# Kernel optimization log

Hardware: AMD Instinct MI355X
Metric: run time of the kernel (lower is better)

## Reference

```python
import jax, jax.numpy as jnp
import numpy as np

NUM_HEADS = 16
NUM_KV_HEADS = 4
FEATURES = 2048
HEAD_DIM = 128
SOFT_CAP = 50.0
WINDOW = 1024
B, T = 2, 2048


def apply_rope(inputs, positions, head_dim, max_wavelength=10000):
    # inputs: [B, T, N, H], positions: [B, T]
    fraction = 2 * jnp.arange(0, head_dim // 2) / head_dim
    timescale = max_wavelength ** fraction  # [H/2]
    sinusoid = positions[..., jnp.newaxis] / timescale[jnp.newaxis, jnp.newaxis, :]  # [B,T,H/2]
    sinusoid = sinusoid[..., jnp.newaxis, :]  # [B,T,1,H/2]
    sin, cos = jnp.sin(sinusoid), jnp.cos(sinusoid)
    first, second = jnp.split(inputs, 2, axis=-1)
    out = jnp.concatenate([first * cos - second * sin, second * cos + first * sin], axis=-1)
    return out.astype(inputs.dtype)


def setup_inputs() -> dict:
    key = jax.random.key(0)
    k1, k2, k3, k4 = jax.random.split(key, 4)
    x = jax.random.normal(k1, (B, T, FEATURES), dtype=jnp.float32)
    segment_pos = jnp.tile(jnp.arange(T, dtype=jnp.int32)[None, :], (B, 1))
    attn_mask = jnp.tril(jnp.ones((T, T), dtype=bool))[None, :, :].repeat(B, axis=0)  # causal [B,T,S]
    std = 0.02
    wq = jax.random.normal(k2, (NUM_HEADS, FEATURES, HEAD_DIM), dtype=jnp.float32) * std
    wkv = jax.random.normal(k3, (2, NUM_KV_HEADS, FEATURES, HEAD_DIM), dtype=jnp.float32) * std
    wvec = jax.random.normal(k4, (NUM_HEADS, HEAD_DIM, FEATURES), dtype=jnp.float32) * std
    return {"x": x, "segment_pos": segment_pos, "attn_mask": attn_mask, "wq": wq, "wkv": wkv, "wvec": wvec}


def reference(x, segment_pos, attn_mask, wq, wkv, wvec):
    # projections
    q = jnp.einsum('BTD,NDH->BTNH', x, wq)                 # [B,T,N,H]
    k, v = jnp.einsum('BSD,CKDH->CBSKH', x, wkv)           # each [B,S,K,H]
    # RoPE + scale
    q = apply_rope(q, segment_pos, HEAD_DIM)
    q = q * jnp.reciprocal(jnp.sqrt(jnp.float32(HEAD_DIM))).astype(q.dtype)
    k = apply_rope(k, segment_pos, HEAD_DIM)
    # GQA logits
    b, t, n, h = q.shape
    g = n // NUM_KV_HEADS
    qg = q.reshape(b, t, NUM_KV_HEADS, g, h)
    logits = jnp.einsum('BTKGH,BSKH->BTKGS', qg, k).reshape(b, t, n, -1)  # [B,T,N,S]
    # soft cap
    logits = jnp.tanh(logits / SOFT_CAP) * SOFT_CAP
    # sliding-window mask combined with causal mask
    ones = jnp.ones_like(attn_mask)
    sliding = jnp.triu(ones, -WINDOW + 1) * jnp.tril(ones, WINDOW - 1)
    mask = sliding * attn_mask  # [B,T,S]
    padded = jnp.where(mask[:, :, None, :], logits, jnp.finfo(logits.dtype).min)
    probs = jax.nn.softmax(padded, axis=-1).astype(k.dtype)
    # GQA weighted values
    pg = probs.reshape(b, t, NUM_KV_HEADS, g, -1)
    enc = jnp.einsum('BTKGS,BSKH->BTKGH', pg, v).reshape(b, t, n, h)
    out = jnp.einsum('BTNH,NHD->BTD', enc, wvec)
    return out
```

## Files before the change

kernel.cpp:

```cpp
#include <hip/hip_runtime.h>
#include <hip/hip_bf16.h>

#define DEVINL static __device__ __forceinline__

typedef __attribute__((ext_vector_type(4))) float f32x4;
typedef __attribute__((ext_vector_type(8))) short bf16x8;

DEVINL short f2bf(float f) {
  __hip_bfloat16 h = __float2bfloat16(f);
  union { __hip_bfloat16 h; short s; } u; u.h = h; return u.s;
}
DEVINL float bf2f(short s) {
  union { unsigned u; float f; } v; v.u = ((unsigned)(unsigned short)s) << 16;
  return v.f;
}
DEVINL float ldf(float x) { return x; }
DEVINL float ldf(short x) { return bf2f(x); }

__global__ void k_cvt(const float* __restrict__ in, short* __restrict__ out, int n4) {
  int i = blockIdx.x * blockDim.x + threadIdx.x;
  if (i >= n4) return;
  const float4 v = reinterpret_cast<const float4*>(in)[i];
  short4 o;
  o.x = f2bf(v.x); o.y = f2bf(v.y); o.z = f2bf(v.z); o.w = f2bf(v.w);
  reinterpret_cast<short4*>(out)[i] = o;
}

template <typename Tin>
__global__ void k_tr(const Tin* __restrict__ in, short* __restrict__ out, int R, int C) {
  __shared__ float tile[32][33];
  const int bz = blockIdx.z;
  const int r0 = blockIdx.y * 32, c0 = blockIdx.x * 32;
  const int tx = threadIdx.x & 31, ty = threadIdx.x >> 5;
  const Tin* ip = in + (size_t)bz * R * C;
  short* op = out + (size_t)bz * R * C;
#pragma unroll
  for (int k = 0; k < 4; k++)
    tile[ty + k * 8][tx] = ldf(ip[(size_t)(r0 + ty + k * 8) * C + c0 + tx]);
  __syncthreads();
#pragma unroll
  for (int k = 0; k < 4; k++)
    op[(size_t)(c0 + ty + k * 8) * R + r0 + tx] = f2bf(tile[tx][ty + k * 8]);
}

__global__ void k_trall(const float* __restrict__ wq, const float* __restrict__ wkv,
                        const float* __restrict__ wvec, short* __restrict__ wall,
                        short* __restrict__ wvecT) {
  __shared__ float tile[32][33];
  const int id = blockIdx.x;
  const float* ip;
  short* op;
  int C, r0, c0;
  if (id < 6144) {
    const int z = id >> 8, rem = id & 255;
    c0 = (rem & 3) * 32;
    r0 = (rem >> 2) * 32;
    C = 128;
    if (z < 16)      ip = wq + (size_t)z * 262144;
    else if (z < 20) ip = wkv + (size_t)(z - 16) * 262144;
    else             ip = wkv + 1048576 + (size_t)(z - 20) * 262144;
    op = wall + (size_t)z * 262144;
  } else {
    const int rem = id - 6144;
    c0 = (rem & 63) * 32;
    r0 = (rem >> 6) * 32;
    C = 2048;
    ip = wvec;
    op = wvecT;
  }
  const int tx = threadIdx.x & 31, ty = threadIdx.x >> 5;
#pragma unroll
  for (int k = 0; k < 4; k++)
    tile[ty + k * 8][tx] = ip[(size_t)(r0 + ty + k * 8) * C + c0 + tx];
  __syncthreads();
#pragma unroll
  for (int k = 0; k < 4; k++)
    op[(size_t)(c0 + ty + k * 8) * 2048 + r0 + tx] = f2bf(tile[tx][ty + k * 8]);
}


#define GBAR __builtin_amdgcn_s_barrier()
#define LGK asm volatile("s_waitcnt lgkmcnt(0)")
#define PR1 __builtin_amdgcn_s_setprio(1)
#define PR0 __builtin_amdgcn_s_setprio(0)
#define VMW { if constexpr (LPA + LPB == 4) asm volatile("s_waitcnt vmcnt(4)");       \
              else if constexpr (LPA + LPB == 3) asm volatile("s_waitcnt vmcnt(3)");  \
              else asm volatile("s_waitcnt vmcnt(2)"); }

template <int LN>
DEVINL void stage(char* dst, const short* src, int K, int tid) {
#pragma unroll
  for (int L = 0; L < LN; L++) {
    const int loc = L * 8192 + tid * 16;
    const int row = loc >> 7;
    const int gsw = ((loc >> 4) & 7) ^ (row & 7);
    __builtin_amdgcn_global_load_lds(
        (const __attribute__((address_space(1))) void*)(src + (size_t)row * K + gsw * 8),
        (__attribute__((address_space(3))) void*)(dst + loc), 16, 0, 0);
  }
}

#define SA(BUF, HALF, KT) \
  stage<LPA>((BUF) + (HALF) * (ABY / 2), Am + (size_t)((HALF) * (BM / 2)) * K + (KT) * 64, K, tid)
#define SB(BUF, HALF, KT) \
  stage<LPB>((BUF) + (HALF) * (BBY / 2), Bn + (size_t)((HALF) * (BN / 2)) * K + (KT) * 64, K, tid)

#define RDA(BUF, IH)                                                                   \
  { _Pragma("unroll")                                                                  \
    for (int kf_ = 0; kf_ < KFN; kf_++) {                                              \
      _Pragma("unroll")                                                                \
      for (int kk_ = 0; kk_ < 2; kk_++) {                                              \
        const int row_ = ((IH) * KFN + kf_) * 32 + wr * 16 + lr;                       \
        a[kf_ * 2 + kk_] = *(const bf16x8*)((BUF) + row_ * 128 +                       \
                                            (((kk_ * 4 + lu) ^ (lr & 7)) << 4));       \
      } } }

#define RDB(BUF, JH, ARR)                                                              \
  { _Pragma("unroll")                                                                  \
    for (int jf_ = 0; jf_ < JFN; jf_++) {                                              \
      _Pragma("unroll")                                                                \
      for (int kk_ = 0; kk_ < 2; kk_++) {                                              \
        const int row_ = ((JH) * JFN + jf_) * 64 + wc * 16 + lr;                       \
        ARR[jf_ * 2 + kk_] = *(const bf16x8*)((BUF) + row_ * 128 +                     \
                                              (((kk_ * 4 + lu) ^ (lr & 7)) << 4));     \
      } } }

#define MF(IH, JH, ARR)                                                                \
  { _Pragma("unroll")                                                                  \
    for (int kf_ = 0; kf_ < KFN; kf_++)                                                \
      { _Pragma("unroll")                                                              \
        for (int jf_ = 0; jf_ < JFN; jf_++)                                            \
          { _Pragma("unroll")                                                          \
            for (int kk_ = 0; kk_ < 2; kk_++)                                          \
              acc[(IH) * KFN + kf_][(JH) * JFN + jf_] =                                \
                  __builtin_amdgcn_mfma_f32_16x16x32_bf16(                             \
                      a[kf_ * 2 + kk_], ARR[jf_ * 2 + kk_],                            \
                      acc[(IH) * KFN + kf_][(JH) * JFN + jf_], 0, 0, 0);               \
          } } }

template <int BM, int BN>
__global__ __launch_bounds__(512, 2) void k_gemm256(
    const short* __restrict__ A, const short* __restrict__ Bt,
    void* __restrict__ Out0, void* __restrict__ Out1,
    int N, int K, int mode) {
  constexpr int LPA = BM / 128;
  constexpr int LPB = BN / 128;
  constexpr int KFN = BM / 64;
  constexpr int JFN = BN / 128;
  constexpr int ABY = BM * 128;
  constexpr int BBY = BN * 128;
  extern __shared__ __align__(16) char sm[];
  char* A0 = sm;
  char* A1 = sm + ABY;
  char* B0 = sm + 2 * ABY;
  char* B1 = sm + 2 * ABY + BBY;
  const int lin = blockIdx.x + gridDim.x * blockIdx.y;
  const int nc = N / BN;
  const int m0 = (lin / nc) * BM, n0 = (lin % nc) * BN;
  const int tid = threadIdx.x, lane = tid & 63, w = tid >> 6;
  const int wr = w & 1, wc = w >> 1;
  const int lr = lane & 15, lu = lane >> 4;
  const short* Am = A + (size_t)m0 * K;
  const short* Bn = Bt + (size_t)n0 * K;
  f32x4 acc[KFN * 2][JFN * 2] = {};
  bf16x8 a[KFN * 2], bJ0[JFN * 2], bJ1[JFN * 2];
  const int NIT = K >> 7;
  const int TMAX = (K >> 6) - 1;

  SA(A0, 0, 0); SB(B0, 1, 0); SA(A0, 1, 0); SB(B0, 0, 0);
  SA(A1, 0, 1); SB(B1, 1, 1);
  VMW; GBAR;

  for (int it = 0; it < NIT; ++it) {
    const int t1 = 2 * it + 1;
    const int t2 = (2 * it + 2 < TMAX) ? 2 * it + 2 : TMAX;
    const int t3 = (2 * it + 3 < TMAX) ? 2 * it + 3 : TMAX;
    RDA(A0, 0); RDB(B0, 0, bJ0); RDB(B0, 1, bJ1); SA(A1, 1, t1); SB(B1, 0, t1);
    GBAR; LGK; PR1; MF(0, 0, bJ0); MF(0, 1, bJ1); PR0; GBAR;
    RDA(A0, 1); SA(A0, 0, t2); SB(B0, 1, t2);
    GBAR; LGK; PR1; MF(1, 1, bJ1); MF(1, 0, bJ0); PR0; VMW; GBAR;
    RDA(A1, 0); RDB(B1, 0, bJ0); RDB(B1, 1, bJ1); SA(A0, 1, t2); SB(B0, 0, t2);
    GBAR; LGK; PR1; MF(0, 0, bJ0); MF(0, 1, bJ1); PR0; GBAR;
    RDA(A1, 1); SA(A1, 0, t3); SB(B1, 1, t3);
    GBAR; LGK; PR1; MF(1, 1, bJ1); MF(1, 0, bJ0); PR0; VMW; GBAR;
  }

  if (mode == 2) {
#pragma unroll
    for (int k = 0; k < KFN * 2; k++)
#pragma unroll
      for (int j = 0; j < JFN * 2; j++)
#pragma unroll
        for (int r = 0; r < 4; r++) {
          const int m = m0 + k * 32 + wr * 16 + lu * 4 + r;
          const int n = n0 + j * 64 + wc * 16 + lr;
          ((float*)Out0)[(size_t)m * N + n] = acc[k][j][r];
        }
  } else {
    const int i_rope = wc * 16 + lr;
    const float inv = __expf(-(float)i_rope * (float)(9.210340371976184 / 64.0));
#pragma unroll
    for (int k = 0; k < KFN * 2; k++) {
      float sn[4], cs[4];
#pragma unroll
      for (int r = 0; r < 4; r++) {
        const int m = m0 + k * 32 + wr * 16 + lu * 4 + r;
        sincosf((float)(m & 2047) * inv, &sn[r], &cs[r]);
      }
#pragma unroll
      for (int u = 0; u < JFN; u++) {
        const int n_lo = n0 + (2 * u) * 64 + wc * 16 + lr;
        const int reg = (n_lo < 2048) ? 0 : ((n_lo < 2560) ? 1 : 2);
#pragma unroll
        for (int r = 0; r < 4; r++) {
          const int m = m0 + k * 32 + wr * 16 + lu * 4 + r;
          const int bb = m >> 11, t = m & 2047;
          float lo = acc[k][2 * u][r], hi = acc[k][2 * u + 1][r];
          if (reg < 2) {
            const float l2 = lo * cs[r] - hi * sn[r];
            const float h2 = hi * cs[r] + lo * sn[r];
            const float sc = (reg == 0) ? 0.08838834764831845f : 1.0f;
            lo = l2 * sc; hi = h2 * sc;
          }
#pragma unroll
          for (int p = 0; p < 2; p++) {
            const int n = n_lo + p * 64;
            const float v = p ? hi : lo;
            if (n < 2048) {
              ((short*)Out0)[(((size_t)(bb * 16 + (n >> 7))) << 18) + t * 128 + (n & 127)] =
                  f2bf(v);
            } else {
              const int nn = n - 2048;
              ((short*)Out1)[(((size_t)(((nn >> 9) * 2 + bb) * 4 + ((nn >> 7) & 3))) << 18) +
                             t * 128 + (nn & 127)] = f2bf(v);
            }
          }
        }
      }
    }
  }
}

__global__ __launch_bounds__(256) void k_attn(
    const short* __restrict__ q, const short* __restrict__ kk,
    const short* __restrict__ vT, short* __restrict__ enc) {
  __shared__ __align__(16) short lK[64 * 128];
  __shared__ __align__(16) short lV[128 * 64];
  __shared__ __align__(16) short lP[4][16 * 64];
  const int bn = blockIdx.x, b = bn >> 4, n = bn & 15, kv = n >> 2;
  const int qt0 = (31 - blockIdx.y) * 64;
  const int tid = threadIdx.x, lane = tid & 63, w = tid >> 6;
  const int lr = lane & 15, lu = lane >> 4;
  const short* qbase = q + (((size_t)(b * 16 + n)) << 18) + (size_t)(qt0 + w * 16) * 128;
  bf16x8 qa[4];
#pragma unroll
  for (int c = 0; c < 4; c++)
    qa[c] = *reinterpret_cast<const bf16x8*>(qbase + lr * 128 + c * 32 + lu * 8);
  f32x4 o[8] = {};
  float lsum = 0.f;
  const short* kbase = kk + (((size_t)(b * 4 + kv)) << 18);
  const short* vbase = vT + (((size_t)(b * 4 + kv)) << 18);
  char* lPw = (char*)lP[w];
  const int tw = qt0 + w * 16;
  const int t_row = tw + lu * 4;
  int st0 = qt0 - 1023; if (st0 < 0) st0 = 0;
  st0 >>= 6;
  const int stE = (qt0 + 63) >> 6;
  for (int st = st0; st <= stE; st++) {
    const int s0 = st << 6;
#pragma unroll
    for (int c = 0; c < 4; c++) {
      const int L = w * 4096 + c * 1024 + lane * 16;
      {
        const int s = L >> 8, slot = (L >> 4) & 15;
        const int sp = slot ^ (s & 7);
        __builtin_amdgcn_global_load_lds(
            (const __attribute__((address_space(1))) void*)(kbase + (size_t)(s0 + s) * 128 + sp * 8),
            (__attribute__((address_space(3))) void*)((char*)lK + L), 16, 0, 0);
      }
      {
        const int h = L >> 7, slot = (L >> 4) & 7;
        const int u = slot ^ (h & 7);
        __builtin_amdgcn_global_load_lds(
            (const __attribute__((address_space(1))) void*)(vbase + (size_t)h * 2048 + s0 + u * 8),
            (__attribute__((address_space(3))) void*)((char*)lV + L), 16, 0, 0);
      }
    }
    __syncthreads();
    f32x4 sc[4];
    __builtin_amdgcn_s_setprio(1);
#pragma unroll
    for (int cg = 0; cg < 4; cg++) {
      sc[cg] = (f32x4){0.f, 0.f, 0.f, 0.f};
      const int s = cg * 16 + lr;
      const int sw = (s & 7) << 4;
#pragma unroll
      for (int c = 0; c < 4; c++) {
        bf16x8 kb = *reinterpret_cast<const bf16x8*>((char*)lK + s * 256 + (((c * 4 + lu) << 4) ^ sw));
        sc[cg] = __builtin_amdgcn_mfma_f32_16x16x32_bf16(kb, qa[c], sc[cg], 0, 0, 0);
      }
    }
    __builtin_amdgcn_s_setprio(0);
    const bool allv = (s0 + 63 <= tw) && (s0 + 1008 >= tw);
    if (allv) {
#pragma unroll
      for (int cg = 0; cg < 4; cg++) {
        float pr[4];
#pragma unroll
        for (int r = 0; r < 4; r++) {
          const float x = sc[cg][r];
          const float cap = __builtin_fmaf(x * x * x, -1.3333333e-4f, x);
          const float p = __expf(cap);
          lsum += p;
          pr[r] = p;
        }
        unsigned w0, w1;
        asm("v_cvt_pk_bf16_f32 %0, %1, %2" : "=v"(w0) : "v"(pr[0]), "v"(pr[1]));
        asm("v_cvt_pk_bf16_f32 %0, %1, %2" : "=v"(w1) : "v"(pr[2]), "v"(pr[3]));
        const int sb = (cg * 16 + lu * 4) << 1;
        *(unsigned*)(lPw + (lr << 7) + (sb ^ ((lr & 7) << 4))) = w0;
        *(unsigned*)(lPw + (lr << 7) + ((sb + 4) ^ ((lr & 7) << 4))) = w1;
      }
    } else {
      const int t = tw + lr;
#pragma unroll
      for (int cg = 0; cg < 4; cg++) {
        float pr[4];
#pragma unroll
        for (int r = 0; r < 4; r++) {
          const int s = s0 + cg * 16 + lu * 4 + r;
          const bool valid = (s <= t) & (s + 1024 > t);
          const float x = sc[cg][r];
          const float cap = __builtin_fmaf(x * x * x, -1.3333333e-4f, x);
          float p = __expf(cap);
          p = valid ? p : 0.f;
          lsum += p;
          pr[r] = p;
        }
        unsigned w0, w1;
        asm("v_cvt_pk_bf16_f32 %0, %1, %2" : "=v"(w0) : "v"(pr[0]), "v"(pr[1]));
        asm("v_cvt_pk_bf16_f32 %0, %1, %2" : "=v"(w1) : "v"(pr[2]), "v"(pr[3]));
        const int sb = (cg * 16 + lu * 4) << 1;
        *(unsigned*)(lPw + (lr << 7) + (sb ^ ((lr & 7) << 4))) = w0;
        *(unsigned*)(lPw + (lr << 7) + ((sb + 4) ^ ((lr & 7) << 4))) = w1;
      }
    }
#pragma unroll
    for (int ks = 0; ks < 2; ks++) {
      const bf16x8 pf = *reinterpret_cast<const bf16x8*>(
          lPw + (lr << 7) + ((ks * 64 + lu * 16) ^ ((lr & 7) << 4)));
      __builtin_amdgcn_s_setprio(1);
#pragma unroll
      for (int oc = 0; oc < 8; oc++) {
        const int h = oc * 16 + lr;
        bf16x8 vb = *reinterpret_cast<const bf16x8*>(
            (char*)lV + h * 128 + (((ks * 4 + lu) << 4) ^ ((h & 7) << 4)));
        o[oc] = __builtin_amdgcn_mfma_f32_16x16x32_bf16(pf, vb, o[oc], 0, 0, 0);
      }
      __builtin_amdgcn_s_setprio(0);
    }
    __syncthreads();
  }
  float tot = lsum;
  tot += __shfl_xor(tot, 16, 64);
  tot += __shfl_xor(tot, 32, 64);
  float rs[4];
#pragma unroll
  for (int r = 0; r < 4; r++)
    rs[r] = 1.f / __shfl(tot, lu * 4 + r, 64);
#pragma unroll
  for (int oc = 0; oc < 8; oc++)
#pragma unroll
    for (int r = 0; r < 4; r++) {
      const int t = t_row + r;
      enc[((size_t)b * 2048 + t) * 2048 + n * 128 + oc * 16 + lr] = f2bf(o[oc][r] * rs[r]);
    }
}

extern "C" void kernel_launch(void* const* d_in, const int* in_sizes, int n_in,
                              void* d_out, int out_size, void* d_ws, size_t ws_size,
                              hipStream_t stream) {
  (void)in_sizes; (void)n_in; (void)out_size; (void)ws_size;
  const float* x    = (const float*)d_in[0];
  const float* wq   = (const float*)d_in[3];
  const float* wkv  = (const float*)d_in[4];
  const float* wvec = (const float*)d_in[5];
  char* ws = (char*)d_ws;
  size_t off = 0;
  short* xbf   = (short*)(ws + off); off += (size_t)8388608 * 2;
  short* wall  = (short*)(ws + off); off += (size_t)3072 * 2048 * 2;
  short* wvecT = (short*)(ws + off); off += (size_t)2048 * 2048 * 2;
  short* qbuf  = (short*)(ws + off); off += (size_t)2 * 16 * 2048 * 128 * 2;
  short* kvbuf = (short*)(ws + off); off += (size_t)2 * 2 * 4 * 2048 * 128 * 2;
  short* vTbuf = (short*)(ws + off); off += (size_t)2 * 4 * 128 * 2048 * 2;
  short* encb  = (short*)(ws + off); off += (size_t)2 * 2048 * 2048 * 2;

  hipFuncSetAttribute(reinterpret_cast<const void*>(&k_gemm256<128, 384>),
                      hipFuncAttributeMaxDynamicSharedMemorySize, 131072);
  hipFuncSetAttribute(reinterpret_cast<const void*>(&k_gemm256<128, 256>),
                      hipFuncAttributeMaxDynamicSharedMemorySize, 98304);

  k_cvt<<<8192, 256, 0, stream>>>(x, xbf, 2097152);
  k_trall<<<10240, 256, 0, stream>>>(wq, wkv, wvec, wall, wvecT);
  k_gemm256<128, 384><<<dim3(32, 8), 512, 131072, stream>>>(xbf, wall, qbuf, kvbuf,
                                                            3072, 2048, 0);
  k_tr<short><<<dim3(4, 64, 8), 256, 0, stream>>>(kvbuf + 2097152, vTbuf, 2048, 128);
  k_attn<<<dim3(32, 32), 256, 0, stream>>>(qbuf, kvbuf, vTbuf, encb);
  k_gemm256<128, 256><<<dim3(32, 8), 512, 98304, stream>>>(encb, wvecT, d_out, nullptr,
                                                           2048, 2048, 2);
}
```

Before: 168.2 us.

## Merge prep kernels, vectorize V transpose, widen attention tiles to 128 queries

Fuses the x conversion and weight transposes into one launch, replaces the generic V transpose with a 64x64 short4-vectorized version, and doubles the attention block to 8 waves covering 128 query rows. The last change shares each loaded K/V tile across twice as many query rows, cutting global and LDS staging traffic per query. In exchange it halves the number of attention blocks, increases per-block LDS and wave count, and adds one extra key tile per block on the causal diagonal.

```diff
diff --git a/kernel.cpp b/kernel.cpp
--- a/kernel.cpp
+++ b/kernel.cpp
@@ -14,45 +14,27 @@
   union { unsigned u; float f; } v; v.u = ((unsigned)(unsigned short)s) << 16;
   return v.f;
 }
-DEVINL float ldf(float x) { return x; }
-DEVINL float ldf(short x) { return bf2f(x); }
-
-__global__ void k_cvt(const float* __restrict__ in, short* __restrict__ out, int n4) {
-  int i = blockIdx.x * blockDim.x + threadIdx.x;
-  if (i >= n4) return;
-  const float4 v = reinterpret_cast<const float4*>(in)[i];
-  short4 o;
-  o.x = f2bf(v.x); o.y = f2bf(v.y); o.z = f2bf(v.z); o.w = f2bf(v.w);
-  reinterpret_cast<short4*>(out)[i] = o;
-}
-
-template <typename Tin>
-__global__ void k_tr(const Tin* __restrict__ in, short* __restrict__ out, int R, int C) {
-  __shared__ float tile[32][33];
-  const int bz = blockIdx.z;
-  const int r0 = blockIdx.y * 32, c0 = blockIdx.x * 32;
-  const int tx = threadIdx.x & 31, ty = threadIdx.x >> 5;
-  const Tin* ip = in + (size_t)bz * R * C;
-  short* op = out + (size_t)bz * R * C;
-#pragma unroll
-  for (int k = 0; k < 4; k++)
-    tile[ty + k * 8][tx] = ldf(ip[(size_t)(r0 + ty + k * 8) * C + c0 + tx]);
-  __syncthreads();
-#pragma unroll
-  for (int k = 0; k < 4; k++)
-    op[(size_t)(c0 + ty + k * 8) * R + r0 + tx] = f2bf(tile[tx][ty + k * 8]);
-}
-
-__global__ void k_trall(const float* __restrict__ wq, const float* __restrict__ wkv,
-                        const float* __restrict__ wvec, short* __restrict__ wall,
-                        short* __restrict__ wvecT) {
+
+__global__ void k_prep(const float* __restrict__ x, const float* __restrict__ wq,
+                       const float* __restrict__ wkv, const float* __restrict__ wvec,
+                       short* __restrict__ xbf, short* __restrict__ wall,
+                       short* __restrict__ wvecT) {
   __shared__ float tile[32][33];
   const int id = blockIdx.x;
+  if (id < 8192) {
+    const int i = id * 256 + threadIdx.x;
+    const float4 v = reinterpret_cast<const float4*>(x)[i];
+    short4 o;
+    o.x = f2bf(v.x); o.y = f2bf(v.y); o.z = f2bf(v.z); o.w = f2bf(v.w);
+    reinterpret_cast<short4*>(xbf)[i] = o;
+    return;
+  }
   const float* ip;
   short* op;
   int C, r0, c0;
-  if (id < 6144) {
-    const int z = id >> 8, rem = id & 255;
+  if (id < 14336) {
+    const int zid = id - 8192;
+    const int z = zid >> 8, rem = zid & 255;
     c0 = (rem & 3) * 32;
     r0 = (rem >> 2) * 32;
     C = 128;
@@ -61,7 +43,7 @@
     else             ip = wkv + 1048576 + (size_t)(z - 20) * 262144;
     op = wall + (size_t)z * 262144;
   } else {
-    const int rem = id - 6144;
+    const int rem = id - 14336;
     c0 = (rem & 63) * 32;
     r0 = (rem >> 6) * 32;
     C = 2048;
@@ -76,6 +58,30 @@
 #pragma unroll
   for (int k = 0; k < 4; k++)
     op[(size_t)(c0 + ty + k * 8) * 2048 + r0 + tx] = f2bf(tile[tx][ty + k * 8]);
+}
+
+__global__ void k_trv(const short* __restrict__ in, short* __restrict__ out) {
+  __shared__ short t[64][66];
+  const int bz = blockIdx.z;
+  const int s0 = blockIdx.y * 64, h0 = blockIdx.x * 64;
+  const int i = threadIdx.x;
+  const int row = i >> 2, q = i & 3;
+  const short* ip = in + (size_t)bz * 262144;
+  short* op = out + (size_t)bz * 262144;
+#pragma unroll
+  for (int j = 0; j < 4; j++) {
+    const int c = q * 16 + j * 4;
+    const short4 v = *reinterpret_cast<const short4*>(ip + (size_t)(s0 + row) * 128 + h0 + c);
+    t[row][c] = v.x; t[row][c + 1] = v.y; t[row][c + 2] = v.z; t[row][c + 3] = v.w;
+  }
+  __syncthreads();
+#pragma unroll
+  for (int j = 0; j < 4; j++) {
+    const int c = q * 16 + j * 4;
+    short4 v;
+    v.x = t[c][row]; v.y = t[c + 1][row]; v.z = t[c + 2][row]; v.w = t[c + 3][row];
+    *reinterpret_cast<short4*>(op + (size_t)(h0 + row) * 2048 + s0 + c) = v;
+  }
 }
 
 
@@ -241,14 +247,14 @@
   }
 }
 
-__global__ __launch_bounds__(256) void k_attn(
+__global__ __launch_bounds__(512) void k_attn(
     const short* __restrict__ q, const short* __restrict__ kk,
     const short* __restrict__ vT, short* __restrict__ enc) {
   __shared__ __align__(16) short lK[64 * 128];
   __shared__ __align__(16) short lV[128 * 64];
-  __shared__ __align__(16) short lP[4][16 * 64];
+  __shared__ __align__(16) short lP[8][16 * 64];
   const int bn = blockIdx.x, b = bn >> 4, n = bn & 15, kv = n >> 2;
-  const int qt0 = (31 - blockIdx.y) * 64;
+  const int qt0 = (15 - blockIdx.y) * 128;
   const int tid = threadIdx.x, lane = tid & 63, w = tid >> 6;
   const int lr = lane & 15, lu = lane >> 4;
   const short* qbase = q + (((size_t)(b * 16 + n)) << 18) + (size_t)(qt0 + w * 16) * 128;
@@ -265,12 +271,12 @@
   const int t_row = tw + lu * 4;
   int st0 = qt0 - 1023; if (st0 < 0) st0 = 0;
   st0 >>= 6;
-  const int stE = (qt0 + 63) >> 6;
+  const int stE = (qt0 + 127) >> 6;
   for (int st = st0; st <= stE; st++) {
     const int s0 = st << 6;
 #pragma unroll
-    for (int c = 0; c < 4; c++) {
-      const int L = w * 4096 + c * 1024 + lane * 16;
+    for (int c = 0; c < 2; c++) {
+      const int L = c * 8192 + tid * 16;
       {
         const int s = L >> 8, slot = (L >> 4) & 15;
         const int sp = slot ^ (s & 7);
@@ -400,12 +406,11 @@
   hipFuncSetAttribute(reinterpret_cast<const void*>(&k_gemm256<128, 256>),
                       hipFuncAttributeMaxDynamicSharedMemorySize, 98304);
 
-  k_cvt<<<8192, 256, 0, stream>>>(x, xbf, 2097152);
-  k_trall<<<10240, 256, 0, stream>>>(wq, wkv, wvec, wall, wvecT);
+  k_prep<<<18432, 256, 0, stream>>>(x, wq, wkv, wvec, xbf, wall, wvecT);
   k_gemm256<128, 384><<<dim3(32, 8), 512, 131072, stream>>>(xbf, wall, qbuf, kvbuf,
                                                             3072, 2048, 0);
-  k_tr<short><<<dim3(4, 64, 8), 256, 0, stream>>>(kvbuf + 2097152, vTbuf, 2048, 128);
-  k_attn<<<dim3(32, 32), 256, 0, stream>>>(qbuf, kvbuf, vTbuf, encb);
+  k_trv<<<dim3(2, 32, 8), 256, 0, stream>>>(kvbuf + 2097152, vTbuf);
+  k_attn<<<dim3(32, 16), 512, 0, stream>>>(qbuf, kvbuf, vTbuf, encb);
   k_gemm256<128, 256><<<dim3(32, 8), 512, 98304, stream>>>(encb, wvecT, d_out, nullptr,
                                                            2048, 2048, 2);
 }
```

Result: faster. 164.8 us (-2.1%).
